# Performance work log

Measured on AMD Instinct MI355X. Metric: run time of the kernel, lower is better.

Reference implementation:

```python
import jax, jax.numpy as jnp
import numpy as np

NUM_HEADS = 8
NUM_LEVELS = 4
NUM_POINTS = 4
EMBED = 256
HEAD_DIM = EMBED // NUM_HEADS
SPATIAL = [(100, 100), (50, 50), (25, 25), (13, 13)]  # (H, W) per level


def _bilinear_sample(val, grid):
    """torch.nn.functional.grid_sample(mode='bilinear', padding_mode='zeros', align_corners=False).
    val: [B, H, W, C], grid: [B, N, 2] with (x, y) in [-1, 1]. Returns [B, N, C]."""
    B, H, W, C = val.shape
    x = (grid[..., 0] + 1.0) * (W * 0.5) - 0.5
    y = (grid[..., 1] + 1.0) * (H * 0.5) - 0.5
    x0 = jnp.floor(x)
    y0 = jnp.floor(y)
    wx1 = x - x0
    wy1 = y - y0
    wx0 = 1.0 - wx1
    wy0 = 1.0 - wy1
    x0i = x0.astype(jnp.int32)
    y0i = y0.astype(jnp.int32)
    valf = val.reshape(B, H * W, C)

    def corner(xi, yi, w):
        valid = (xi >= 0) & (xi < W) & (yi >= 0) & (yi < H)
        idx = jnp.clip(yi, 0, H - 1) * W + jnp.clip(xi, 0, W - 1)
        v = jnp.take_along_axis(valf, idx[..., None], axis=1)  # [B, N, C]
        return v * (w * valid)[..., None]

    return (corner(x0i, y0i, wx0 * wy0) + corner(x0i + 1, y0i, wx1 * wy0)
            + corner(x0i, y0i + 1, wx0 * wy1) + corner(x0i + 1, y0i + 1, wx1 * wy1))


def setup_inputs() -> dict:
    key = jax.random.key(0)
    ks = jax.random.split(key, 12)
    bs, nq = 4, 6000
    nv = sum(h * w for h, w in SPATIAL)
    s = 0.02
    return {
        "query": jax.random.normal(ks[0], (bs, nq, EMBED), jnp.float32),
        "value": jax.random.normal(ks[1], (bs, nv, EMBED), jnp.float32),
        "reference_points": jax.random.uniform(ks[2], (bs, nq, NUM_LEVELS, 2), jnp.float32),
        "W_off": jax.random.normal(ks[3], (EMBED, NUM_HEADS * NUM_LEVELS * NUM_POINTS * 2), jnp.float32) * s,
        "b_off": jax.random.normal(ks[4], (NUM_HEADS * NUM_LEVELS * NUM_POINTS * 2,), jnp.float32),
        "W_attn": jax.random.normal(ks[5], (EMBED, NUM_HEADS * NUM_LEVELS * NUM_POINTS), jnp.float32) * s,
        "b_attn": jnp.zeros((NUM_HEADS * NUM_LEVELS * NUM_POINTS,), jnp.float32),
        "W_val": jax.random.normal(ks[6], (EMBED, EMBED), jnp.float32) * s,
        "b_val": jnp.zeros((EMBED,), jnp.float32),
        "W_out": jax.random.normal(ks[7], (EMBED, EMBED), jnp.float32) * s,
        "b_out": jnp.zeros((EMBED,), jnp.float32),
        "spatial_shapes": jnp.asarray(np.array(SPATIAL, dtype=np.int32)),
    }


def reference(query, value, reference_points, W_off, b_off, W_attn, b_attn,
              W_val, b_val, W_out, b_out, spatial_shapes):
    shapes = [(int(h), int(w)) for h, w in np.asarray(spatial_shapes)]
    bs, nq, _ = query.shape
    nv = value.shape[1]

    v = (value @ W_val + b_val).reshape(bs, nv, NUM_HEADS, HEAD_DIM)
    offsets = (query @ W_off + b_off).reshape(bs, nq, NUM_HEADS, NUM_LEVELS, NUM_POINTS, 2)
    aw = (query @ W_attn + b_attn).reshape(bs, nq, NUM_HEADS, NUM_LEVELS * NUM_POINTS)
    aw = jax.nn.softmax(aw, axis=-1).reshape(bs, nq, NUM_HEADS, NUM_LEVELS, NUM_POINTS)

    # offset normalizer is [W, H] per level
    norm = jnp.asarray([[w, h] for h, w in shapes], dtype=query.dtype)  # [L, 2]
    loc = reference_points[:, :, None, :, None, :] + offsets / norm[None, None, None, :, None, :]
    grids = 2.0 * loc - 1.0  # [bs, nq, H, L, P, 2]
    # -> [bs*H, nq*P, 2] per level
    grids = jnp.transpose(grids, (0, 2, 1, 3, 4, 5)).reshape(bs * NUM_HEADS, nq, NUM_LEVELS, NUM_POINTS, 2)

    v_bh = jnp.transpose(v, (0, 2, 1, 3)).reshape(bs * NUM_HEADS, nv, HEAD_DIM)
    sampled = []
    start = 0
    for l, (H_, W_) in enumerate(shapes):
        val_l = v_bh[:, start:start + H_ * W_].reshape(bs * NUM_HEADS, H_, W_, HEAD_DIM)
        grid_l = grids[:, :, l].reshape(bs * NUM_HEADS, nq * NUM_POINTS, 2)
        s_l = _bilinear_sample(val_l, grid_l).reshape(bs * NUM_HEADS, nq, NUM_POINTS, HEAD_DIM)
        sampled.append(s_l)
        start += H_ * W_
    sampled = jnp.stack(sampled, axis=2)  # [bs*H, nq, L, P, c]

    aw_bh = jnp.transpose(aw, (0, 2, 1, 3, 4)).reshape(bs * NUM_HEADS, nq, NUM_LEVELS, NUM_POINTS)
    out = (sampled * aw_bh[..., None]).sum(axis=(2, 3))  # [bs*H, nq, c]
    out = out.reshape(bs, NUM_HEADS, nq, HEAD_DIM).transpose(0, 2, 1, 3).reshape(bs, nq, EMBED)
    out = out @ W_out + b_out
    return out + query
```

## Files before the change

### kernel.cpp

```cpp
#include <hip/hip_runtime.h>
#include <hip/hip_bf16.h>

#define BS 4
#define NQ 6000
#define NV 13294
#define NH 8
#define HD 32
#define EMB 256
#define MV (BS * NV)
#define MQ (BS * NQ)

typedef __attribute__((ext_vector_type(8))) short short8;
typedef __attribute__((ext_vector_type(4))) float floatx4;

__device__ __constant__ float LVL_DIM[4] = {100.f, 50.f, 25.f, 13.f};

__device__ inline unsigned short bf16bits(float f) {
  __hip_bfloat16 h = __float2bfloat16(f);
  return *reinterpret_cast<unsigned short*>(&h);
}
__device__ inline unsigned int pk2bf(float lo, float hi) {
  return (unsigned int)bf16bits(lo) | ((unsigned int)bf16bits(hi) << 16);
}
__device__ inline float bflo(unsigned int u) { return __uint_as_float(u << 16); }
__device__ inline float bfhi(unsigned int u) { return __uint_as_float(u & 0xffff0000u); }

#define LDSTR 40
#define TILEU (128 * LDSTR)

__global__ __launch_bounds__(256) void wtrans_kernel(
    const float* __restrict__ W_val, const float* __restrict__ W_off,
    const float* __restrict__ W_attn, const float* __restrict__ W_out,
    unsigned short* __restrict__ Wt_val, unsigned short* __restrict__ Wt_qcat,
    unsigned short* __restrict__ Wt_out) {
  __shared__ float tile[32][33];
  const int b = blockIdx.x;
  const int x = threadIdx.x & 31, ty = threadIdx.x >> 5;

  const float* src;
  unsigned short* dst;
  int k0, n0;
  if (b < 64) {
    src = W_val;
    dst = Wt_val;
    k0 = (b >> 3) * 32;
    n0 = (b & 7) * 32;
  } else if (b < 128) {
    const int bb = b - 64;
    src = W_off;
    dst = Wt_qcat;
    k0 = (bb >> 3) * 32;
    n0 = (bb & 7) * 32;
  } else if (b < 160) {
    const int bb = b - 128;
    src = W_attn;
    dst = Wt_qcat + 256 * EMB;
    k0 = (bb >> 2) * 32;
    n0 = (bb & 3) * 32;
#pragma unroll
    for (int i = 0; i < 4; ++i)
      tile[ty + 8 * i][x] = src[(size_t)(k0 + ty + 8 * i) * 128 + n0 + x];
    __syncthreads();
#pragma unroll
    for (int i = 0; i < 4; ++i)
      dst[(size_t)(n0 + ty + 8 * i) * EMB + k0 + x] =
          bf16bits(tile[x][ty + 8 * i]);
    return;
  } else {
    const int bb = b - 160;
    src = W_out;
    dst = Wt_out;
    k0 = (bb >> 3) * 32;
    n0 = (bb & 7) * 32;
  }
#pragma unroll
  for (int i = 0; i < 4; ++i)
    tile[ty + 8 * i][x] = src[(size_t)(k0 + ty + 8 * i) * 256 + n0 + x];
  __syncthreads();
#pragma unroll
  for (int i = 0; i < 4; ++i)
    dst[(size_t)(n0 + ty + 8 * i) * EMB + k0 + x] = bf16bits(tile[x][ty + 8 * i]);
}

__device__ inline void loadA32(const float* __restrict__ A, int M, int m0,
                               int k0, int tid, float4 ra[4]) {
  const int r = tid >> 1, kh = (tid & 1) * 16;
  const int row = m0 + r;
  if (row < M) {
    const float* src = A + (size_t)row * EMB + k0 + kh;
#pragma unroll
    for (int j = 0; j < 4; ++j) ra[j] = *(const float4*)(src + 4 * j);
  } else {
#pragma unroll
    for (int j = 0; j < 4; ++j) ra[j] = make_float4(0.f, 0.f, 0.f, 0.f);
  }
}
__device__ inline void storeA32(unsigned short* lds, int tid,
                                const float4 ra[4]) {
  const int r = tid >> 1, kh = (tid & 1) * 16;
  unsigned short* dst = lds + r * LDSTR + kh;
  uint4 u0, u1;
  u0.x = pk2bf(ra[0].x, ra[0].y);
  u0.y = pk2bf(ra[0].z, ra[0].w);
  u0.z = pk2bf(ra[1].x, ra[1].y);
  u0.w = pk2bf(ra[1].z, ra[1].w);
  u1.x = pk2bf(ra[2].x, ra[2].y);
  u1.y = pk2bf(ra[2].z, ra[2].w);
  u1.z = pk2bf(ra[3].x, ra[3].y);
  u1.w = pk2bf(ra[3].z, ra[3].w);
  *(uint4*)(dst) = u0;
  *(uint4*)(dst + 8) = u1;
}
__device__ inline void loadBb(const unsigned short* __restrict__ B, int NB,
                              int n0, int k0, int tid, uint4 rb[2]) {
  const int r = tid >> 1, kh = (tid & 1) * 16;
  const int row = n0 + r;
  if (row < NB) {
    const unsigned short* src = B + (size_t)row * EMB + k0 + kh;
    rb[0] = *(const uint4*)(src);
    rb[1] = *(const uint4*)(src + 8);
  } else {
    rb[0] = make_uint4(0, 0, 0, 0);
    rb[1] = make_uint4(0, 0, 0, 0);
  }
}
__device__ inline void storeBb(unsigned short* lds, int tid,
                               const uint4 rb[2]) {
  const int r = tid >> 1, kh = (tid & 1) * 16;
  unsigned short* dst = lds + r * LDSTR + kh;
  *(uint4*)(dst) = rb[0];
  *(uint4*)(dst + 8) = rb[1];
}

__device__ inline void mfma_step32(const unsigned short* ldsA,
                                   const unsigned short* ldsB, int wm, int wn,
                                   int lane, floatx4 acc[4][4]) {
  const unsigned short* ap =
      ldsA + (wm * 64 + (lane & 15)) * LDSTR + (lane >> 4) * 8;
  const unsigned short* bp =
      ldsB + (wn * 64 + (lane & 15)) * LDSTR + (lane >> 4) * 8;
  short8 af[4], bfr[4];
#pragma unroll
  for (int t = 0; t < 4; ++t) {
    af[t] = *(const short8*)(ap + t * 16 * LDSTR);
    bfr[t] = *(const short8*)(bp + t * 16 * LDSTR);
  }
#pragma unroll
  for (int mt = 0; mt < 4; ++mt)
#pragma unroll
    for (int nt = 0; nt < 4; ++nt)
      acc[mt][nt] = __builtin_amdgcn_mfma_f32_16x16x32_bf16(af[mt], bfr[nt],
                                                            acc[mt][nt], 0, 0, 0);
}

__device__ inline void gemm_loop32_f32A(const float* __restrict__ A, int M,
                                        int m0,
                                        const unsigned short* __restrict__ B,
                                        int NB, int n0, unsigned short* lds,
                                        int tid, int wm, int wn, int lane,
                                        floatx4 acc[4][4]) {
  unsigned short* bufA[2] = {lds, lds + 2 * TILEU};
  unsigned short* bufB[2] = {lds + TILEU, lds + 3 * TILEU};
  float4 sa[2][4];
  uint4 sb[2][2];
  loadA32(A, M, m0, 0, tid, sa[0]);
  loadBb(B, NB, n0, 0, tid, sb[0]);
  loadA32(A, M, m0, 32, tid, sa[1]);
  loadBb(B, NB, n0, 32, tid, sb[1]);
  storeA32(bufA[0], tid, sa[0]);
  storeBb(bufB[0], tid, sb[0]);
  __syncthreads();
#pragma unroll
  for (int k = 0; k < 8; ++k) {
    const int cur = k & 1, nxt = cur ^ 1;
    if (k + 2 < 8) {
      loadA32(A, M, m0, (k + 2) * 32, tid, sa[k & 1]);
      loadBb(B, NB, n0, (k + 2) * 32, tid, sb[k & 1]);
    }
    if (k + 1 < 8) {
      storeA32(bufA[nxt], tid, sa[(k + 1) & 1]);
      storeBb(bufB[nxt], tid, sb[(k + 1) & 1]);
    }
    mfma_step32(bufA[cur], bufB[cur], wm, wn, lane, acc);
    __syncthreads();
  }
}

__device__ inline void gemm_loop32_bf16A(const unsigned short* __restrict__ A,
                                         int M, int m0,
                                         const unsigned short* __restrict__ B,
                                         int NB, int n0, unsigned short* lds,
                                         int tid, int wm, int wn, int lane,
                                         floatx4 acc[4][4]) {
  unsigned short* bufA[2] = {lds, lds + 2 * TILEU};
  unsigned short* bufB[2] = {lds + TILEU, lds + 3 * TILEU};
  uint4 sa[2][2], sb[2][2];
  loadBb(A, M, m0, 0, tid, sa[0]);
  loadBb(B, NB, n0, 0, tid, sb[0]);
  loadBb(A, M, m0, 32, tid, sa[1]);
  loadBb(B, NB, n0, 32, tid, sb[1]);
  storeBb(bufA[0], tid, sa[0]);
  storeBb(bufB[0], tid, sb[0]);
  __syncthreads();
#pragma unroll
  for (int k = 0; k < 8; ++k) {
    const int cur = k & 1, nxt = cur ^ 1;
    if (k + 2 < 8) {
      loadBb(A, M, m0, (k + 2) * 32, tid, sa[k & 1]);
      loadBb(B, NB, n0, (k + 2) * 32, tid, sb[k & 1]);
    }
    if (k + 1 < 8) {
      storeBb(bufA[nxt], tid, sa[(k + 1) & 1]);
      storeBb(bufB[nxt], tid, sb[(k + 1) & 1]);
    }
    mfma_step32(bufA[cur], bufB[cur], wm, wn, lane, acc);
    __syncthreads();
  }
}

__global__ __launch_bounds__(256, 2) void vproj_kernel(
    const float* __restrict__ value, const unsigned short* __restrict__ Wt_val,
    const float* __restrict__ b_val, unsigned short* __restrict__ vbh) {
  __shared__ unsigned short lds[4 * TILEU];
  const int tid = threadIdx.x, lane = tid & 63, w = tid >> 6;
  const int wm = w >> 1, wn = w & 1;
  floatx4 acc[4][4];
  const floatx4 zero = {0.f, 0.f, 0.f, 0.f};
#pragma unroll
  for (int i2 = 0; i2 < 4; i2++)
#pragma unroll
    for (int j = 0; j < 4; j++) acc[i2][j] = zero;
  const int quad = lane >> 4, cl = lane & 15;

  const int chunk = blockIdx.x >> 4, i = blockIdx.x & 15;
  const int m0 = (chunk * 8 + (i & 7)) * 128;
  const int n0 = (i >> 3) * 128;
  gemm_loop32_f32A(value, MV, m0, Wt_val, 256, n0, lds, tid, wm, wn, lane,
                   acc);
#pragma unroll
  for (int mt = 0; mt < 4; ++mt) {
#pragma unroll
    for (int r = 0; r < 4; ++r) {
      const int row = m0 + wm * 64 + mt * 16 + quad * 4 + r;
      if (row < MV) {
        const int b = row / NV, n = row - b * NV;
#pragma unroll
        for (int nt = 0; nt < 4; ++nt) {
          const int c = n0 + wn * 64 + nt * 16 + cl;
          const int h = c >> 5, d = c & 31;
          vbh[(((size_t)(b * NH + h)) * NV + n) * HD + d] =
              bf16bits(acc[mt][nt][r] + b_val[c]);
        }
      }
    }
  }
}

__global__ __launch_bounds__(256, 2) void qproj_kernel(
    const float* __restrict__ query, const unsigned short* __restrict__ Wt_qcat,
    const float* __restrict__ refpts, const float* __restrict__ b_off,
    const float* __restrict__ b_attn, float* __restrict__ locbuf,
    float* __restrict__ awbuf) {
  __shared__ unsigned short lds[4 * TILEU];
  const int tid = threadIdx.x, lane = tid & 63, w = tid >> 6;
  const int wm = w >> 1, wn = w & 1;
  floatx4 acc[4][4];
  const floatx4 zero = {0.f, 0.f, 0.f, 0.f};
#pragma unroll
  for (int i2 = 0; i2 < 4; i2++)
#pragma unroll
    for (int j = 0; j < 4; j++) acc[i2][j] = zero;
  const int quad = lane >> 4, cl = lane & 15;

  const int bid = blockIdx.x;
  const int chunk = bid / 24, i = bid % 24;
  const int m_idx = chunk * 8 + (i & 7);
  if (m_idx >= 188) return;
  const int m0 = m_idx * 128;
  const int n0 = (i >> 3) * 128;
  gemm_loop32_f32A(query, MQ, m0, Wt_qcat, 384, n0, lds, tid, wm, wn, lane,
                   acc);
  if (n0 < 256) {
#pragma unroll
    for (int mt = 0; mt < 4; ++mt) {
#pragma unroll
      for (int r = 0; r < 4; ++r) {
        const int row = m0 + wm * 64 + mt * 16 + quad * 4 + r;
        if (row < MQ) {
#pragma unroll
          for (int nt = 0; nt < 4; ++nt) {
            const int c = n0 + wn * 64 + nt * 16 + cl;
            const int xy = c & 1, l = (c >> 3) & 3;
            const float dim = LVL_DIM[l];
            const float ref = refpts[(size_t)row * 8 + l * 2 + xy];
            locbuf[(size_t)row * 256 + c] =
                ref * dim + acc[mt][nt][r] + b_off[c] - 0.5f;
          }
        }
      }
    }
  } else {
#pragma unroll
    for (int mt = 0; mt < 4; ++mt) {
#pragma unroll
      for (int r = 0; r < 4; ++r) {
        const int row = m0 + wm * 64 + mt * 16 + quad * 4 + r;
        if (row < MQ) {
#pragma unroll
          for (int nt = 0; nt < 4; ++nt) {
            const int ca = wn * 64 + nt * 16 + cl;
            float v = acc[mt][nt][r] + b_attn[ca];
            float m = v;
            m = fmaxf(m, __shfl_xor(m, 1));
            m = fmaxf(m, __shfl_xor(m, 2));
            m = fmaxf(m, __shfl_xor(m, 4));
            m = fmaxf(m, __shfl_xor(m, 8));
            float e = __expf(v - m);
            float s = e;
            s += __shfl_xor(s, 1);
            s += __shfl_xor(s, 2);
            s += __shfl_xor(s, 4);
            s += __shfl_xor(s, 8);
            awbuf[(size_t)row * 128 + ca] = e / s;
          }
        }
      }
    }
  }
}

__global__ __launch_bounds__(256, 4) void sample_kernel(
    const unsigned short* __restrict__ vbh, const float* __restrict__ locbuf,
    const float* __restrict__ awbuf, unsigned short* __restrict__ sampledb) {
  const int blk = blockIdx.x;
  const int t = blk >> 3;
  const int quarter = t / 375;
  const int j = t - quarter * 375;
  const int slice = (blk & 7) * 4 + quarter;
  const int h = slice & 7;
  const int w = threadIdx.x >> 6;
  const int lane = threadIdx.x & 63;
  const int r0 = (slice >> 3) * NQ + j * 16 + w * 4;
  const int g = lane >> 2;
  const int d8 = lane & 3;
  const int l = g >> 2;

  const int W_ = (l < 2) ? ((l == 0) ? 100 : 50) : ((l == 2) ? 25 : 13);
  const int START = (l < 2) ? ((l == 0) ? 0 : 10000) : ((l == 2) ? 12500 : 13125);
  const unsigned int* base =
      (const unsigned int*)vbh + ((size_t)slice * NV + START) * 16 + d8 * 4;

  float acc[4][8];
#pragma unroll
  for (int rr = 0; rr < 4; ++rr) {
    const int row = r0 + rr;
    const float2 xy =
        *(const float2*)(locbuf + (size_t)row * 256 + h * 32 + g * 2);
    const float wgt = awbuf[(size_t)row * 128 + h * 16 + g];

    const float fx = floorf(xy.x), fy = floorf(xy.y);
    const int x0 = (int)fx, y0 = (int)fy;
    const float wx1 = xy.x - fx, wy1 = xy.y - fy;
    const float wx0 = 1.f - wx1, wy0 = 1.f - wy1;
    const int x0c = min(max(x0, 0), W_ - 1), x1c = min(max(x0 + 1, 0), W_ - 1);
    const int y0c = min(max(y0, 0), W_ - 1), y1c = min(max(y0 + 1, 0), W_ - 1);
    const float mx0 = ((unsigned)x0 < (unsigned)W_) ? wx0 : 0.f;
    const float mx1 = ((unsigned)(x0 + 1) < (unsigned)W_) ? wx1 : 0.f;
    const float my0 = ((unsigned)y0 < (unsigned)W_) ? wy0 : 0.f;
    const float my1 = ((unsigned)(y0 + 1) < (unsigned)W_) ? wy1 : 0.f;
    const float wy0w = wgt * my0, wy1w = wgt * my1;
    const float w00 = wy0w * mx0, w01 = wy0w * mx1;
    const float w10 = wy1w * mx0, w11 = wy1w * mx1;

    const int rb0 = y0c * W_, rb1 = y1c * W_;
    const uint4 u00 = *(const uint4*)(base + (size_t)(rb0 + x0c) * 16);
    const uint4 u01 = *(const uint4*)(base + (size_t)(rb0 + x1c) * 16);
    const uint4 u10 = *(const uint4*)(base + (size_t)(rb1 + x0c) * 16);
    const uint4 u11 = *(const uint4*)(base + (size_t)(rb1 + x1c) * 16);
    const unsigned int* p00 = &u00.x;
    const unsigned int* p01 = &u01.x;
    const unsigned int* p10 = &u10.x;
    const unsigned int* p11 = &u11.x;
#pragma unroll
    for (int k = 0; k < 4; ++k) {
      acc[rr][2 * k] = w00 * bflo(p00[k]) + w01 * bflo(p01[k]) +
                       w10 * bflo(p10[k]) + w11 * bflo(p11[k]);
      acc[rr][2 * k + 1] = w00 * bfhi(p00[k]) + w01 * bfhi(p01[k]) +
                           w10 * bfhi(p10[k]) + w11 * bfhi(p11[k]);
    }
  }

  const bool b0 = (lane >> 2) & 1;
  const bool b1 = (lane >> 3) & 1;
  const bool b2 = (lane >> 4) & 1;
#pragma unroll
  for (int rr = 0; rr < 4; ++rr) {
    float* v = acc[rr];
#pragma unroll
    for (int jj = 0; jj < 4; ++jj) {
      float lo = v[jj], hi = v[jj + 4];
      float recv = __shfl_xor(b0 ? lo : hi, 4);
      v[jj] = (b0 ? hi : lo) + recv;
    }
#pragma unroll
    for (int jj = 0; jj < 2; ++jj) {
      float lo = v[jj], hi = v[jj + 2];
      float recv = __shfl_xor(b1 ? lo : hi, 8);
      v[jj] = (b1 ? hi : lo) + recv;
    }
    {
      float lo = v[0], hi = v[1];
      float recv = __shfl_xor(b2 ? lo : hi, 16);
      v[0] = (b2 ? hi : lo) + recv;
    }
    v[0] += __shfl_xor(v[0], 32);
  }

  const int dim = d8 * 8 + (b0 ? 4 : 0) + (b1 ? 2 : 0) + (b2 ? 1 : 0);
  const bool hi = (lane >= 32);
  const float v0 = hi ? acc[1][0] : acc[0][0];
  const float v1 = hi ? acc[3][0] : acc[2][0];
  const int row0 = r0 + (hi ? 1 : 0);
  const int row1 = r0 + 2 + (hi ? 1 : 0);
  sampledb[(size_t)row0 * EMB + h * 32 + dim] = bf16bits(v0);
  sampledb[(size_t)row1 * EMB + h * 32 + dim] = bf16bits(v1);
}

__global__ __launch_bounds__(256, 2) void oproj_kernel(
    const unsigned short* __restrict__ sampledb,
    const unsigned short* __restrict__ Wt, const float* __restrict__ b_out,
    const float* __restrict__ query, float* __restrict__ out) {
  __shared__ unsigned short lds[4 * TILEU];
  const int tid = threadIdx.x, lane = tid & 63, w = tid >> 6;
  const int wm = w >> 1, wn = w & 1;
  const int chunk = blockIdx.x >> 4, i = blockIdx.x & 15;
  const int m_idx = chunk * 8 + (i & 7);
  if (m_idx >= 188) return;
  const int m0 = m_idx * 128;
  const int n0 = (i >> 3) * 128;
  floatx4 acc[4][4];
  const floatx4 zero = {0.f, 0.f, 0.f, 0.f};
#pragma unroll
  for (int i2 = 0; i2 < 4; i2++)
#pragma unroll
    for (int j = 0; j < 4; j++) acc[i2][j] = zero;

  gemm_loop32_bf16A(sampledb, MQ, m0, Wt, 256, n0, lds, tid, wm, wn, lane,
                    acc);

  const int quad = lane >> 4, cl = lane & 15;
#pragma unroll
  for (int mt = 0; mt < 4; ++mt) {
#pragma unroll
    for (int r = 0; r < 4; ++r) {
      const int row = m0 + wm * 64 + mt * 16 + quad * 4 + r;
      if (row < MQ) {
#pragma unroll
        for (int nt = 0; nt < 4; ++nt) {
          const int c = n0 + wn * 64 + nt * 16 + cl;
          out[(size_t)row * EMB + c] =
              acc[mt][nt][r] + b_out[c] + query[(size_t)row * EMB + c];
        }
      }
    }
  }
}

extern "C" void kernel_launch(void* const* d_in, const int* in_sizes, int n_in,
                              void* d_out, int out_size, void* d_ws,
                              size_t ws_size, hipStream_t stream) {
  const float* query  = (const float*)d_in[0];
  const float* value  = (const float*)d_in[1];
  const float* refpts = (const float*)d_in[2];
  const float* W_off  = (const float*)d_in[3];
  const float* b_off  = (const float*)d_in[4];
  const float* W_attn = (const float*)d_in[5];
  const float* b_attn = (const float*)d_in[6];
  const float* W_val  = (const float*)d_in[7];
  const float* b_val  = (const float*)d_in[8];
  const float* W_out  = (const float*)d_in[9];
  const float* b_out  = (const float*)d_in[10];
  float* out = (float*)d_out;

  char* ws = (char*)d_ws;
  unsigned short* vbh = (unsigned short*)ws;
  float* locbuf = (float*)(ws + 27226112);
  float* awbuf = (float*)(ws + 51802112);
  unsigned short* sampledb = (unsigned short*)(ws + 64090112);
  unsigned short* Wt_val = (unsigned short*)(ws + 76378112);
  unsigned short* Wt_qcat = (unsigned short*)(ws + 76509184);
  unsigned short* Wt_out = (unsigned short*)(ws + 76705792);

  wtrans_kernel<<<224, 256, 0, stream>>>(W_val, W_off, W_attn, W_out, Wt_val,
                                         Wt_qcat, Wt_out);
  vproj_kernel<<<832, 256, 0, stream>>>(value, Wt_val, b_val, vbh);
  qproj_kernel<<<576, 256, 0, stream>>>(query, Wt_qcat, refpts, b_off, b_attn,
                                        locbuf, awbuf);
  sample_kernel<<<12000, 256, 0, stream>>>(vbh, locbuf, awbuf, sampledb);
  oproj_kernel<<<384, 256, 0, stream>>>(sampledb, Wt_out, b_out, query, out);
}
```

Baseline: 233.9 us.

## Split softmax into separate kernel and pack sampling math into float2 vectors

Moves the per-head softmax over attention logits out of the qproj GEMM epilogue, where it used shuffle reductions, into a new lightweight kernel in which each thread normalizes one 16-element row with vector loads. The bilinear sampling accumulation and its first butterfly reduction stages are rewritten with two-wide float vectors so the compiler can emit packed FP32 math. The split adds one extra launch and an extra read and write of the attention buffer, in exchange for a lighter GEMM epilogue and a cheaper sampling inner loop.

After: 241.1 us. +3.1%, slower.

```diff
diff --git a/kernel.cpp b/kernel.cpp
--- a/kernel.cpp
+++ b/kernel.cpp
@@ -12,6 +12,7 @@
 
 typedef __attribute__((ext_vector_type(8))) short short8;
 typedef __attribute__((ext_vector_type(4))) float floatx4;
+typedef __attribute__((ext_vector_type(2))) float f32x2;
 
 __device__ __constant__ float LVL_DIM[4] = {100.f, 50.f, 25.f, 13.f};
 
@@ -24,6 +25,15 @@
 }
 __device__ inline float bflo(unsigned int u) { return __uint_as_float(u << 16); }
 __device__ inline float bfhi(unsigned int u) { return __uint_as_float(u & 0xffff0000u); }
+__device__ inline f32x2 splat2(float s) {
+  f32x2 r; r[0] = s; r[1] = s; return r;
+}
+__device__ inline f32x2 bfpair(unsigned int u) {
+  f32x2 r;
+  r[0] = __uint_as_float(u << 16);
+  r[1] = __uint_as_float(u & 0xffff0000u);
+  return r;
+}
 
 #define LDSTR 40
 #define TILEU (128 * LDSTR)
@@ -309,24 +319,44 @@
 #pragma unroll
           for (int nt = 0; nt < 4; ++nt) {
             const int ca = wn * 64 + nt * 16 + cl;
-            float v = acc[mt][nt][r] + b_attn[ca];
-            float m = v;
-            m = fmaxf(m, __shfl_xor(m, 1));
-            m = fmaxf(m, __shfl_xor(m, 2));
-            m = fmaxf(m, __shfl_xor(m, 4));
-            m = fmaxf(m, __shfl_xor(m, 8));
-            float e = __expf(v - m);
-            float s = e;
-            s += __shfl_xor(s, 1);
-            s += __shfl_xor(s, 2);
-            s += __shfl_xor(s, 4);
-            s += __shfl_xor(s, 8);
-            awbuf[(size_t)row * 128 + ca] = e / s;
+            awbuf[(size_t)row * 128 + ca] = acc[mt][nt][r] + b_attn[ca];
           }
         }
       }
     }
   }
+}
+
+__global__ __launch_bounds__(256) void smax_kernel(float* __restrict__ awbuf) {
+  const int rh = blockIdx.x * 256 + threadIdx.x;
+  float4 a0 = *(const float4*)(awbuf + (size_t)rh * 16);
+  float4 a1 = *(const float4*)(awbuf + (size_t)rh * 16 + 4);
+  float4 a2 = *(const float4*)(awbuf + (size_t)rh * 16 + 8);
+  float4 a3 = *(const float4*)(awbuf + (size_t)rh * 16 + 12);
+  float m0 = fmaxf(fmaxf(a0.x, a0.y), fmaxf(a0.z, a0.w));
+  float m1 = fmaxf(fmaxf(a1.x, a1.y), fmaxf(a1.z, a1.w));
+  float m2 = fmaxf(fmaxf(a2.x, a2.y), fmaxf(a2.z, a2.w));
+  float m3 = fmaxf(fmaxf(a3.x, a3.y), fmaxf(a3.z, a3.w));
+  const float m = fmaxf(fmaxf(m0, m1), fmaxf(m2, m3));
+  a0.x = __expf(a0.x - m); a0.y = __expf(a0.y - m);
+  a0.z = __expf(a0.z - m); a0.w = __expf(a0.w - m);
+  a1.x = __expf(a1.x - m); a1.y = __expf(a1.y - m);
+  a1.z = __expf(a1.z - m); a1.w = __expf(a1.w - m);
+  a2.x = __expf(a2.x - m); a2.y = __expf(a2.y - m);
+  a2.z = __expf(a2.z - m); a2.w = __expf(a2.w - m);
+  a3.x = __expf(a3.x - m); a3.y = __expf(a3.y - m);
+  a3.z = __expf(a3.z - m); a3.w = __expf(a3.w - m);
+  const float s = (a0.x + a0.y + a0.z + a0.w) + (a1.x + a1.y + a1.z + a1.w) +
+                  (a2.x + a2.y + a2.z + a2.w) + (a3.x + a3.y + a3.z + a3.w);
+  const float inv = 1.f / s;
+  a0.x *= inv; a0.y *= inv; a0.z *= inv; a0.w *= inv;
+  a1.x *= inv; a1.y *= inv; a1.z *= inv; a1.w *= inv;
+  a2.x *= inv; a2.y *= inv; a2.z *= inv; a2.w *= inv;
+  a3.x *= inv; a3.y *= inv; a3.z *= inv; a3.w *= inv;
+  *(float4*)(awbuf + (size_t)rh * 16) = a0;
+  *(float4*)(awbuf + (size_t)rh * 16 + 4) = a1;
+  *(float4*)(awbuf + (size_t)rh * 16 + 8) = a2;
+  *(float4*)(awbuf + (size_t)rh * 16 + 12) = a3;
 }
 
 __global__ __launch_bounds__(256, 4) void sample_kernel(
@@ -350,7 +380,7 @@
   const unsigned int* base =
       (const unsigned int*)vbh + ((size_t)slice * NV + START) * 16 + d8 * 4;
 
-  float acc[4][8];
+  f32x2 facc[4][4];
 #pragma unroll
   for (int rr = 0; rr < 4; ++rr) {
     const int row = r0 + rr;
@@ -369,8 +399,8 @@
     const float my0 = ((unsigned)y0 < (unsigned)W_) ? wy0 : 0.f;
     const float my1 = ((unsigned)(y0 + 1) < (unsigned)W_) ? wy1 : 0.f;
     const float wy0w = wgt * my0, wy1w = wgt * my1;
-    const float w00 = wy0w * mx0, w01 = wy0w * mx1;
-    const float w10 = wy1w * mx0, w11 = wy1w * mx1;
+    const f32x2 w00 = splat2(wy0w * mx0), w01 = splat2(wy0w * mx1);
+    const f32x2 w10 = splat2(wy1w * mx0), w11 = splat2(wy1w * mx1);
 
     const int rb0 = y0c * W_, rb1 = y1c * W_;
     const uint4 u00 = *(const uint4*)(base + (size_t)(rb0 + x0c) * 16);
@@ -383,43 +413,50 @@
     const unsigned int* p11 = &u11.x;
 #pragma unroll
     for (int k = 0; k < 4; ++k) {
-      acc[rr][2 * k] = w00 * bflo(p00[k]) + w01 * bflo(p01[k]) +
-                       w10 * bflo(p10[k]) + w11 * bflo(p11[k]);
-      acc[rr][2 * k + 1] = w00 * bfhi(p00[k]) + w01 * bfhi(p01[k]) +
-                           w10 * bfhi(p10[k]) + w11 * bfhi(p11[k]);
+      facc[rr][k] = w00 * bfpair(p00[k]) + w01 * bfpair(p01[k]) +
+                    w10 * bfpair(p10[k]) + w11 * bfpair(p11[k]);
     }
   }
 
   const bool b0 = (lane >> 2) & 1;
   const bool b1 = (lane >> 3) & 1;
   const bool b2 = (lane >> 4) & 1;
+  float out[4];
 #pragma unroll
   for (int rr = 0; rr < 4; ++rr) {
-    float* v = acc[rr];
-#pragma unroll
-    for (int jj = 0; jj < 4; ++jj) {
-      float lo = v[jj], hi = v[jj + 4];
-      float recv = __shfl_xor(b0 ? lo : hi, 4);
-      v[jj] = (b0 ? hi : lo) + recv;
-    }
+    f32x2* f = facc[rr];
 #pragma unroll
     for (int jj = 0; jj < 2; ++jj) {
-      float lo = v[jj], hi = v[jj + 2];
-      float recv = __shfl_xor(b1 ? lo : hi, 8);
-      v[jj] = (b1 ? hi : lo) + recv;
+      f32x2 lo = f[jj], hi = f[jj + 2];
+      f32x2 keep = b0 ? hi : lo;
+      f32x2 send = b0 ? lo : hi;
+      f32x2 recv;
+      recv[0] = __shfl_xor(send[0], 4);
+      recv[1] = __shfl_xor(send[1], 4);
+      f[jj] = keep + recv;
     }
     {
-      float lo = v[0], hi = v[1];
+      f32x2 lo = f[0], hi = f[1];
+      f32x2 keep = b1 ? hi : lo;
+      f32x2 send = b1 ? lo : hi;
+      f32x2 recv;
+      recv[0] = __shfl_xor(send[0], 8);
+      recv[1] = __shfl_xor(send[1], 8);
+      f[0] = keep + recv;
+    }
+    {
+      float lo = f[0][0], hi = f[0][1];
       float recv = __shfl_xor(b2 ? lo : hi, 16);
-      v[0] = (b2 ? hi : lo) + recv;
-    }
-    v[0] += __shfl_xor(v[0], 32);
+      float v = (b2 ? hi : lo) + recv;
+      v += __shfl_xor(v, 32);
+      out[rr] = v;
+    }
   }
 
   const int dim = d8 * 8 + (b0 ? 4 : 0) + (b1 ? 2 : 0) + (b2 ? 1 : 0);
   const bool hi = (lane >= 32);
-  const float v0 = hi ? acc[1][0] : acc[0][0];
-  const float v1 = hi ? acc[3][0] : acc[2][0];
+  const float v0 = hi ? out[1] : out[0];
+  const float v1 = hi ? out[3] : out[2];
   const int row0 = r0 + (hi ? 1 : 0);
   const int row1 = r0 + 2 + (hi ? 1 : 0);
   sampledb[(size_t)row0 * EMB + h * 32 + dim] = bf16bits(v0);
@@ -496,6 +533,7 @@
   vproj_kernel<<<832, 256, 0, stream>>>(value, Wt_val, b_val, vbh);
   qproj_kernel<<<576, 256, 0, stream>>>(query, Wt_qcat, refpts, b_off, b_attn,
                                         locbuf, awbuf);
+  smax_kernel<<<750, 256, 0, stream>>>(awbuf);
   sample_kernel<<<12000, 256, 0, stream>>>(vbh, locbuf, awbuf, sampledb);
   oproj_kernel<<<384, 256, 0, stream>>>(sampledb, Wt_out, b_out, query, out);
 }
```
